# Kernel tuning notes

Hardware: AMD Instinct MI355X
Metric: run time of the kernel (lower is better)

Reference implementation:

```python
import jax, jax.numpy as jnp
import numpy as np

# Config from Hyperparameters / __init__ args
B, S, D = 2, 2048, 512
H, KV, HD = 8, 4, 64          # num_heads, num_kv_heads, head_dim = D // H
ROPE_BASE = 10000.0
QK_GAIN_INIT = 1.5
EPS = 1e-6


def setup_inputs() -> dict:
    key = jax.random.key(0)
    k0, k1, k2, k3, k4 = jax.random.split(key, 5)
    std = 0.02
    return {
        "x": jax.random.normal(k0, (B, S, D), dtype=jnp.float32),
        "wq": jax.random.normal(k1, (H * HD, D), dtype=jnp.float32) * std,
        "wk": jax.random.normal(k2, (KV * HD, D), dtype=jnp.float32) * std,
        "wv": jax.random.normal(k3, (KV * HD, D), dtype=jnp.float32) * std,
        "wo": jax.random.normal(k4, (D, H * HD), dtype=jnp.float32) * std,
        "qk_gain": jnp.asarray(QK_GAIN_INIT, dtype=jnp.float32),
    }


def _rope_tables(seq_len, head_dim, base, dtype):
    inv_freq = 1.0 / (base ** (jnp.arange(0, head_dim, 2, dtype=jnp.float32) / head_dim))
    t = jnp.arange(seq_len, dtype=jnp.float32)
    freqs = t[:, None] * inv_freq[None, :]              # [S, HD/2]
    return jnp.cos(freqs).astype(dtype)[None, None], jnp.sin(freqs).astype(dtype)[None, None]


def _apply_rotary(x, cos, sin):
    # matches apply_rotary_emb: split halves, rotate
    half = x.shape[-1] // 2
    x1, x2 = x[..., :half], x[..., half:]
    return jnp.concatenate([x1 * cos + x2 * sin, x1 * (-sin) + x2 * cos], axis=-1)


def _rms_norm(u):
    return u * jax.lax.rsqrt(jnp.mean(u * u, axis=-1, keepdims=True) + EPS)


def reference(x, wq, wk, wv, wo, qk_gain):
    b, s, d = x.shape
    # fused-style QKV projections (CastedLinear, no bias)
    q = (x @ wq.T).reshape(b, s, H, HD).transpose(0, 2, 1, 3)    # [B,H,S,HD]
    k = (x @ wk.T).reshape(b, s, KV, HD).transpose(0, 2, 1, 3)   # [B,KV,S,HD]
    v = (x @ wv.T).reshape(b, s, KV, HD).transpose(0, 2, 1, 3)   # [B,KV,S,HD]

    cos, sin = _rope_tables(s, HD, ROPE_BASE, x.dtype)
    q = _apply_rotary(q, cos, sin)
    k = _apply_rotary(k, cos, sin)

    # QK RMS-norm with learnable gain (init 1.5) on q
    q = _rms_norm(q) * qk_gain
    k = _rms_norm(k)

    # GQA: expand KV heads to H query heads
    rep = H // KV
    k = jnp.repeat(k, rep, axis=1)   # [B,H,S,HD]
    v = jnp.repeat(v, rep, axis=1)

    scale = 1.0 / np.sqrt(HD)
    scores = jnp.einsum("bhqd,bhkd->bhqk", q, k) * scale         # [B,H,S,S]
    causal = jnp.tril(jnp.ones((s, s), dtype=bool))
    scores = jnp.where(causal, scores, jnp.finfo(scores.dtype).min)
    attn = jax.nn.softmax(scores, axis=-1)
    out = jnp.einsum("bhqk,bhkd->bhqd", attn, v)                 # [B,H,S,HD]
    out = out.transpose(0, 2, 1, 3).reshape(b, s, H * HD)
    return out @ wo.T
```

## Files before the change

### kernel.cpp

```cpp
#include <hip/hip_runtime.h>
#include <math.h>

#define B_ 2
#define S_ 2048
#define D_ 512
#define H_ 8
#define KV_ 4
#define HD_ 64

typedef __attribute__((ext_vector_type(8))) short bf16x8;
typedef __attribute__((ext_vector_type(4))) short bf16x4;
typedef __attribute__((ext_vector_type(4))) float f32x4;
typedef __attribute__((ext_vector_type(16))) float f32x16;
typedef __attribute__((ext_vector_type(4))) unsigned u32x4;

static __device__ __forceinline__ unsigned short f2bf(float f) {
    union { float f; unsigned u; } v; v.f = f;
    unsigned r = v.u + 0x7FFFu + ((v.u >> 16) & 1);
    return (unsigned short)(r >> 16);
}

__global__ __launch_bounds__(256) void convert_pack_kernel(
    const float* __restrict__ x, const float* __restrict__ wq, const float* __restrict__ wk,
    const float* __restrict__ wv, const float* __restrict__ wo,
    unsigned short* __restrict__ xb, unsigned short* __restrict__ wqkv_b,
    unsigned short* __restrict__ wo_b, float* __restrict__ cosT, float* __restrict__ sinT) {
    if (blockIdx.x >= 2816) {
        int idx = (blockIdx.x - 2816) * 256 + threadIdx.x;
        int s = idx >> 5;
        int i = idx & 31;
        float invf = 1.0f / powf(10000.0f, (float)(2 * i) / (float)HD_);
        double a = (double)((float)s * invf);
        cosT[idx] = (float)cos(a);
        sinT[idx] = (float)sin(a);
        return;
    }
    int i4 = blockIdx.x * blockDim.x + threadIdx.x;
    int e = i4 * 4;
    const float* src;
    unsigned short* dst;
    if (e < 2097152)      { src = x + e;               dst = xb + e; }
    else if (e < 2359296) { src = wq + (e - 2097152);  dst = wqkv_b + (e - 2097152); }
    else if (e < 2490368) { src = wk + (e - 2359296);  dst = wqkv_b + (e - 2097152); }
    else if (e < 2621440) { src = wv + (e - 2490368);  dst = wqkv_b + (e - 2097152); }
    else                  { src = wo + (e - 2621440);  dst = wo_b + (e - 2621440); }
    float4 v = *(const float4*)src;
    bf16x4 o;
    o[0] = (short)f2bf(v.x); o[1] = (short)f2bf(v.y);
    o[2] = (short)f2bf(v.z); o[3] = (short)f2bf(v.w);
    *(bf16x4*)dst = o;
}

template <int EPI, typename OutT>
__global__ __launch_bounds__(256) void gemm_mfma(
    const unsigned short* __restrict__ A, const unsigned short* __restrict__ Bw,
    OutT* __restrict__ Y, int K, int ldy,
    const float* __restrict__ cosT, const float* __restrict__ sinT,
    const float* __restrict__ gainp) {
    __shared__ unsigned short As[128 * 32];
    __shared__ unsigned short Bs[128 * 32];
    const int bn = blockIdx.x * 128;
    const int bm = blockIdx.y * 128;
    const int t = threadIdx.x;
    const int w = t >> 6, l = t & 63;
    const int g = l >> 4, c = l & 15;
    const int wr = w >> 1, wc = w & 1;
    f32x4 acc[4][4] = {};
    const int lrow = l >> 2;
    const int lcol = (l & 3) * 8;
    for (int k0 = 0; k0 < K; k0 += 32) {
#pragma unroll
        for (int r = 0; r < 2; ++r) {
            int ci = w * 2 + r;
            const unsigned short* ga = A + (size_t)(bm + ci * 16 + lrow) * K + k0 + lcol;
            __builtin_amdgcn_global_load_lds(
                (const __attribute__((address_space(1))) void*)ga,
                (__attribute__((address_space(3))) void*)(As + ci * 512), 16, 0, 0);
            const unsigned short* gb = Bw + (size_t)(bn + ci * 16 + lrow) * K + k0 + lcol;
            __builtin_amdgcn_global_load_lds(
                (const __attribute__((address_space(1))) void*)gb,
                (__attribute__((address_space(3))) void*)(Bs + ci * 512), 16, 0, 0);
        }
        __syncthreads();
        bf16x8 av[4], bv[4];
#pragma unroll
        for (int i = 0; i < 4; ++i)
            av[i] = *(const bf16x8*)(As + (wr * 64 + i * 16 + c) * 32 + g * 8);
#pragma unroll
        for (int j = 0; j < 4; ++j)
            bv[j] = *(const bf16x8*)(Bs + (wc * 64 + j * 16 + c) * 32 + g * 8);
#pragma unroll
        for (int i = 0; i < 4; ++i)
#pragma unroll
            for (int j = 0; j < 4; ++j)
                acc[i][j] = __builtin_amdgcn_mfma_f32_16x16x32_bf16(av[i], bv[j], acc[i][j], 0, 0, 0);
        __syncthreads();
    }
    if constexpr (EPI == 2) {
        const float gv = *gainp;
        const float hscale = ((bn + wc * 64) < 512) ? gv : 1.0f;
#pragma unroll
        for (int i = 0; i < 4; ++i) {
#pragma unroll
            for (int r = 0; r < 4; ++r) {
                int row = bm + wr * 64 + i * 16 + g * 4 + r;
                int s = row & (S_ - 1);
                float c0 = cosT[s * 32 + c],      s0 = sinT[s * 32 + c];
                float c1 = cosT[s * 32 + c + 16], s1 = sinT[s * 32 + c + 16];
                float x1a = acc[i][0][r], x1b = acc[i][1][r];
                float x2a = acc[i][2][r], x2b = acc[i][3][r];
                float y1a = x1a * c0 + x2a * s0, y2a = x2a * c0 - x1a * s0;
                float y1b = x1b * c1 + x2b * s1, y2b = x2b * c1 - x1b * s1;
                float ss = y1a * y1a + y2a * y2a + y1b * y1b + y2b * y2b;
                ss += __shfl_xor(ss, 1, 64);
                ss += __shfl_xor(ss, 2, 64);
                ss += __shfl_xor(ss, 4, 64);
                ss += __shfl_xor(ss, 8, 64);
                float sc = rsqrtf(ss * (1.0f / 64.0f) + 1e-6f) * hscale;
                unsigned short* yr = (unsigned short*)Y + (size_t)row * ldy + bn + wc * 64 + c;
                yr[0]  = f2bf(y1a * sc);
                yr[16] = f2bf(y1b * sc);
                yr[32] = f2bf(y2a * sc);
                yr[48] = f2bf(y2b * sc);
            }
        }
    } else {
#pragma unroll
        for (int i = 0; i < 4; ++i)
#pragma unroll
            for (int j = 0; j < 4; ++j)
#pragma unroll
                for (int r = 0; r < 4; ++r) {
                    int row = bm + wr * 64 + i * 16 + g * 4 + r;
                    int col = bn + wc * 64 + j * 16 + c;
                    float v = acc[i][j][r];
                    if constexpr (EPI == 1)
                        Y[(size_t)row * ldy + col] = (OutT)f2bf(v);
                    else
                        Y[(size_t)row * ldy + col] = v;
                }
    }
}

#define SWZF(row) ((((row) + ((row) >> 3)) & 7) << 4)

__global__ __launch_bounds__(256, 3) void attn_mfma(const unsigned short* __restrict__ qkv,
                                                    const unsigned short* __restrict__ vt,
                                                    unsigned short* __restrict__ aout) {
    __shared__ alignas(128) char smem[32768];

    const int bid = blockIdx.x;
    const int bh = bid & 15;
    const int qt = 31 - (bid >> 4);
    const int hh = bh & 7;
    const int b = bh >> 3;
    const int kvh = hh >> 1;

    const int t = threadIdx.x;
    const int w = t >> 6;
    const int l = t & 63;
    const int wq = w >> 1;
    const int wk = w & 1;
    const int hl = l >> 5;
    const int l31 = l & 31;

    const int row0 = t >> 3;
    const int row1 = (256 + t) >> 3;
    const int seg = l & 7;
    const int off0 = (seg * 16) ^ SWZF(row0);
    const int off1 = (seg * 16) ^ SWZF(row1);
    const int cb0 = w * 1024;
    const int cb1 = 4096 + w * 1024;

    bf16x8 qf[4];
    {
        const unsigned short* qrow =
            qkv + (size_t)(b * S_ + qt * 64 + wq * 32 + l31) * 768 + hh * 64 + hl * 8;
#pragma unroll
        for (int kd = 0; kd < 4; ++kd)
            qf[kd] = *(const bf16x8*)(qrow + kd * 16);
    }

    const char* kb = (const char*)qkv + ((size_t)(b * S_)) * 1536 + 1024 + kvh * 128;
    const char* vb = (const char*)vt + ((size_t)(kvh * 64)) * 8192 + (size_t)(b * S_) * 2;

#define STAGE(kt_, bufi_)                                                                        \
    do {                                                                                         \
        const char* ks_ = kb + (size_t)(kt_) * 64 * 1536;                                        \
        const char* vs_ = vb + (size_t)(kt_) * 128;                                              \
        char* kd_ = smem + (bufi_)*8192;                                                         \
        char* vd_ = smem + 16384 + (bufi_)*8192;                                                 \
        __builtin_amdgcn_global_load_lds(                                                        \
            (const __attribute__((address_space(1))) void*)(ks_ + (size_t)row0 * 1536 + off0),   \
            (__attribute__((address_space(3))) void*)(kd_ + cb0), 16, 0, 0);                     \
        __builtin_amdgcn_global_load_lds(                                                        \
            (const __attribute__((address_space(1))) void*)(ks_ + (size_t)row1 * 1536 + off1),   \
            (__attribute__((address_space(3))) void*)(kd_ + cb1), 16, 0, 0);                     \
        __builtin_amdgcn_global_load_lds(                                                        \
            (const __attribute__((address_space(1))) void*)(vs_ + (size_t)row0 * 8192 + off0),   \
            (__attribute__((address_space(3))) void*)(vd_ + cb0), 16, 0, 0);                     \
        __builtin_amdgcn_global_load_lds(                                                        \
            (const __attribute__((address_space(1))) void*)(vs_ + (size_t)row1 * 8192 + off1),   \
            (__attribute__((address_space(3))) void*)(vd_ + cb1), 16, 0, 0);                     \
    } while (0)

    STAGE(0, 0);
    __syncthreads();

    float l_part = 0.0f;
    f32x16 o_acc[2] = {};
    const float LS = 0.125f * 1.4426950408889634f;
    const float SH = 6.0f * 1.4426950408889634f;

    int buf = 0;
    for (int kt = 0; kt <= qt; ++kt) {
        if (kt < qt) STAGE(kt + 1, buf ^ 1);
        const char* KsB = smem + buf * 8192;
        const char* VtB = smem + 16384 + buf * 8192;
        const bool diag = (kt == qt);

        if (!(diag && wk > wq)) {
            f32x16 s_acc = {};
            {
                int arow = wk * 32 + l31;
                int af = SWZF(arow);
                __builtin_amdgcn_s_setprio(1);
#pragma unroll
                for (int kd = 0; kd < 4; ++kd) {
                    bf16x8 afr = *(const bf16x8*)(KsB + arow * 128 + ((kd * 32 + hl * 16) ^ af));
                    s_acc = __builtin_amdgcn_mfma_f32_32x32x16_bf16(afr, qf[kd], s_acc, 0, 0, 0);
                }
                __builtin_amdgcn_s_setprio(0);
            }
            bf16x8 vf[2][2];
#pragma unroll
            for (int nd = 0; nd < 2; ++nd) {
                int vr = nd * 32 + l31;
                int fv = SWZF(vr);
#pragma unroll
                for (int m = 0; m < 2; ++m)
                    vf[nd][m] = *(const bf16x8*)(VtB + vr * 128 + ((wk * 64 + m * 32 + hl * 16) ^ fv));
            }
            float p[16];
            if (diag && wk == wq) {
#pragma unroll
                for (int idx = 0; idx < 16; ++idx) {
                    int keyin = 4 * hl + 8 * (idx >> 2) + (idx & 3);
                    float e = exp2f(s_acc[idx] * LS - SH);
                    p[idx] = (keyin <= l31) ? e : 0.0f;
                }
            } else {
#pragma unroll
                for (int idx = 0; idx < 16; ++idx)
                    p[idx] = exp2f(s_acc[idx] * LS - SH);
            }
#pragma unroll
            for (int idx = 0; idx < 16; ++idx) l_part += p[idx];
            unsigned pw[8];
#pragma unroll
            for (int s = 0; s < 4; ++s)
#pragma unroll
                for (int j = 0; j < 2; ++j)
                    asm("v_cvt_pk_bf16_f32 %0, %1, %2"
                        : "=v"(pw[s * 2 + j])
                        : "v"(p[4 * s + 2 * j]), "v"(p[4 * s + 2 * j + 1]));
#pragma unroll
            for (int m = 0; m < 2; ++m) {
                asm volatile("v_permlane32_swap_b32 %0, %1" : "+v"(pw[4 * m + 0]), "+v"(pw[4 * m + 2]));
                asm volatile("v_permlane32_swap_b32 %0, %1" : "+v"(pw[4 * m + 1]), "+v"(pw[4 * m + 3]));
            }
            __builtin_amdgcn_s_setprio(1);
#pragma unroll
            for (int m = 0; m < 2; ++m) {
                u32x4 fu = {pw[4 * m + 0], pw[4 * m + 1], pw[4 * m + 2], pw[4 * m + 3]};
                bf16x8 pfr = *(bf16x8*)&fu;
#pragma unroll
                for (int nd = 0; nd < 2; ++nd)
                    o_acc[nd] = __builtin_amdgcn_mfma_f32_32x32x16_bf16(pfr, vf[nd][m], o_acc[nd], 0, 0, 0);
            }
            __builtin_amdgcn_s_setprio(0);
        }
        __syncthreads();
        buf ^= 1;
    }
#undef STAGE

    float* Os = (float*)smem;
    float* Ls = (float*)(smem + 16384);
    float lsum = l_part + __shfl_xor(l_part, 32, 64);
    if (hl == 0) Ls[wk * 64 + wq * 32 + l31] = lsum;
    if (wk == 0) {
#pragma unroll
        for (int nd = 0; nd < 2; ++nd)
#pragma unroll
            for (int reg = 0; reg < 16; ++reg) {
                int qrow = 4 * hl + 8 * (reg >> 2) + (reg & 3);
                Os[(wq * 32 + qrow) * 64 + nd * 32 + l31] = o_acc[nd][reg];
            }
    }
    __syncthreads();
    if (wk == 1) {
        unsigned short* ob = aout + ((size_t)(b * S_ + qt * 64 + wq * 32)) * 512 + hh * 64;
#pragma unroll
        for (int reg = 0; reg < 16; ++reg) {
            int qrow = 4 * hl + 8 * (reg >> 2) + (reg & 3);
            float ltot = Ls[wq * 32 + qrow] + Ls[64 + wq * 32 + qrow];
            float inv = __builtin_amdgcn_rcpf(ltot);
#pragma unroll
            for (int nd = 0; nd < 2; ++nd) {
                float val = (o_acc[nd][reg] + Os[(wq * 32 + qrow) * 64 + nd * 32 + l31]) * inv;
                ob[(size_t)qrow * 512 + nd * 32 + l31] = f2bf(val);
            }
        }
    }
}

extern "C" void kernel_launch(void* const* d_in, const int* in_sizes, int n_in,
                              void* d_out, int out_size, void* d_ws, size_t ws_size,
                              hipStream_t stream) {
    const float* x    = (const float*)d_in[0];
    const float* wq   = (const float*)d_in[1];
    const float* wk   = (const float*)d_in[2];
    const float* wv   = (const float*)d_in[3];
    const float* wo   = (const float*)d_in[4];
    const float* gain = (const float*)d_in[5];
    float* out = (float*)d_out;

    char* ws = (char*)d_ws;
    unsigned short* qkv    = (unsigned short*)(ws);
    unsigned short* vt     = (unsigned short*)(ws + (size_t)6  * 1024 * 1024);
    unsigned short* aout   = (unsigned short*)(ws + (size_t)8  * 1024 * 1024);
    unsigned short* xb     = (unsigned short*)(ws + (size_t)12 * 1024 * 1024);
    unsigned short* wqkv_b = (unsigned short*)(ws + (size_t)16 * 1024 * 1024);
    unsigned short* wo_b   = (unsigned short*)(ws + (size_t)17 * 1024 * 1024);
    float* cosT            = (float*)(ws + (size_t)18 * 1024 * 1024);
    float* sinT            = cosT + (size_t)S_ * (HD_ / 2);

    convert_pack_kernel<<<3072, 256, 0, stream>>>(x, wq, wk, wv, wo, xb, wqkv_b, wo_b,
                                                  cosT, sinT);
    gemm_mfma<2, unsigned short><<<dim3(6, 32), 256, 0, stream>>>(
        xb, wqkv_b, qkv, 512, 768, cosT, sinT, gain);
    gemm_mfma<1, unsigned short><<<dim3(32, 2), 256, 0, stream>>>(
        wqkv_b + 768 * 512, xb, vt, 512, 4096, nullptr, nullptr, nullptr);
    attn_mfma<<<16 * (S_ / 64), 256, 0, stream>>>(qkv, vt, aout);
    gemm_mfma<0, float><<<dim3(4, 32), 256, 0, stream>>>(
        aout, wo_b, out, 512, 512, nullptr, nullptr, nullptr);
}
```

Measured before the change: 79.16 us.

## Split causal attention KV range into chunks and merge QKV/V-transpose GEMM launches

Attention work for each query tile is split into chunks of up to 8 KV tiles, so long causal rows run across several blocks. Partial unnormalized outputs and row sums go to a workspace, and a new combine kernel adds them and normalizes. The softmax shift is fixed, so partials can be summed directly. The QKV GEMM and the V-transpose GEMM are merged into one launch, which removes a launch and lets both fill the GPU together. In exchange there is extra fp32 partial traffic and an additional kernel launch.

```diff
diff --git a/kernel.cpp b/kernel.cpp
--- a/kernel.cpp
+++ b/kernel.cpp
@@ -52,15 +52,12 @@
 }
 
 template <int EPI, typename OutT>
-__global__ __launch_bounds__(256) void gemm_mfma(
+static __device__ __forceinline__ void gemm_body(
     const unsigned short* __restrict__ A, const unsigned short* __restrict__ Bw,
-    OutT* __restrict__ Y, int K, int ldy,
+    OutT* __restrict__ Y, int K, int ldy, int bn, int bm,
+    unsigned short* As, unsigned short* Bs,
     const float* __restrict__ cosT, const float* __restrict__ sinT,
     const float* __restrict__ gainp) {
-    __shared__ unsigned short As[128 * 32];
-    __shared__ unsigned short Bs[128 * 32];
-    const int bn = blockIdx.x * 128;
-    const int bm = blockIdx.y * 128;
     const int t = threadIdx.x;
     const int w = t >> 6, l = t & 63;
     const int g = l >> 4, c = l & 15;
@@ -142,16 +139,52 @@
     }
 }
 
+__global__ __launch_bounds__(256) void gemm_proj_fused(
+    const unsigned short* __restrict__ xb, const unsigned short* __restrict__ wqkv_b,
+    unsigned short* __restrict__ qkv, unsigned short* __restrict__ vt,
+    const float* __restrict__ cosT, const float* __restrict__ sinT,
+    const float* __restrict__ gainp) {
+    __shared__ unsigned short As[128 * 32];
+    __shared__ unsigned short Bs[128 * 32];
+    int bid = blockIdx.x;
+    if (bid < 192) {
+        int bx = bid % 6, by = bid / 6;
+        gemm_body<2, unsigned short>(xb, wqkv_b, qkv, 512, 768, bx * 128, by * 128,
+                                     As, Bs, cosT, sinT, gainp);
+    } else {
+        int b2 = bid - 192;
+        int bx = b2 & 31, by = b2 >> 5;
+        gemm_body<1, unsigned short>(wqkv_b + 768 * 512, xb, vt, 512, 4096, bx * 128, by * 128,
+                                     As, Bs, nullptr, nullptr, nullptr);
+    }
+}
+
+__global__ __launch_bounds__(256) void gemm_out(
+    const unsigned short* __restrict__ A, const unsigned short* __restrict__ Bw,
+    float* __restrict__ Y) {
+    __shared__ unsigned short As[128 * 32];
+    __shared__ unsigned short Bs[128 * 32];
+    gemm_body<0, float>(A, Bw, Y, 512, 512, blockIdx.x % 4 * 128, blockIdx.x / 4 * 128,
+                        As, Bs, nullptr, nullptr, nullptr);
+}
+
 #define SWZF(row) ((((row) + ((row) >> 3)) & 7) << 4)
 
 __global__ __launch_bounds__(256, 3) void attn_mfma(const unsigned short* __restrict__ qkv,
                                                     const unsigned short* __restrict__ vt,
-                                                    unsigned short* __restrict__ aout) {
+                                                    unsigned short* __restrict__ aout,
+                                                    float* __restrict__ pO,
+                                                    float* __restrict__ pL) {
     __shared__ alignas(128) char smem[32768];
 
-    const int bid = blockIdx.x;
-    const int bh = bid & 15;
-    const int qt = 31 - (bid >> 4);
+    const int slot = blockIdx.x >> 4;
+    const int bh = blockIdx.x & 15;
+    int qt = 31, acc = 0;
+    while (acc + (qt >> 3) + 1 <= slot) { acc += (qt >> 3) + 1; --qt; }
+    const int part = slot - acc;
+    const int np = (qt >> 3) + 1;
+    const int kt0 = part * 8;
+    const int kt1 = min(kt0 + 8, qt + 1);
     const int hh = bh & 7;
     const int b = bh >> 3;
     const int kvh = hh >> 1;
@@ -204,7 +237,7 @@
             (__attribute__((address_space(3))) void*)(vd_ + cb1), 16, 0, 0);                     \
     } while (0)
 
-    STAGE(0, 0);
+    STAGE(kt0, 0);
     __syncthreads();
 
     float l_part = 0.0f;
@@ -213,8 +246,8 @@
     const float SH = 6.0f * 1.4426950408889634f;
 
     int buf = 0;
-    for (int kt = 0; kt <= qt; ++kt) {
-        if (kt < qt) STAGE(kt + 1, buf ^ 1);
+    for (int kt = kt0; kt < kt1; ++kt) {
+        if (kt + 1 < kt1) STAGE(kt + 1, buf ^ 1);
         const char* KsB = smem + buf * 8192;
         const char* VtB = smem + 16384 + buf * 8192;
         const bool diag = (kt == qt);
@@ -300,18 +333,73 @@
     }
     __syncthreads();
     if (wk == 1) {
-        unsigned short* ob = aout + ((size_t)(b * S_ + qt * 64 + wq * 32)) * 512 + hh * 64;
-#pragma unroll
-        for (int reg = 0; reg < 16; ++reg) {
-            int qrow = 4 * hl + 8 * (reg >> 2) + (reg & 3);
-            float ltot = Ls[wq * 32 + qrow] + Ls[64 + wq * 32 + qrow];
-            float inv = __builtin_amdgcn_rcpf(ltot);
-#pragma unroll
-            for (int nd = 0; nd < 2; ++nd) {
-                float val = (o_acc[nd][reg] + Os[(wq * 32 + qrow) * 64 + nd * 32 + l31]) * inv;
-                ob[(size_t)qrow * 512 + nd * 32 + l31] = f2bf(val);
+        if (np == 1) {
+            unsigned short* ob = aout + ((size_t)(b * S_ + qt * 64 + wq * 32)) * 512 + hh * 64;
+#pragma unroll
+            for (int reg = 0; reg < 16; ++reg) {
+                int qrow = 4 * hl + 8 * (reg >> 2) + (reg & 3);
+                float ltot = Ls[wq * 32 + qrow] + Ls[64 + wq * 32 + qrow];
+                float inv = __builtin_amdgcn_rcpf(ltot);
+#pragma unroll
+                for (int nd = 0; nd < 2; ++nd) {
+                    float val = (o_acc[nd][reg] + Os[(wq * 32 + qrow) * 64 + nd * 32 + l31]) * inv;
+                    ob[(size_t)qrow * 512 + nd * 32 + l31] = f2bf(val);
+                }
+            }
+        } else {
+            float* po = pO + (size_t)blockIdx.x * 4096;
+            float* pl = pL + (size_t)blockIdx.x * 64;
+#pragma unroll
+            for (int reg = 0; reg < 16; ++reg) {
+                int qrow = 4 * hl + 8 * (reg >> 2) + (reg & 3);
+                float ltot = Ls[wq * 32 + qrow] + Ls[64 + wq * 32 + qrow];
+                if (l31 == 0) pl[wq * 32 + qrow] = ltot;
+#pragma unroll
+                for (int nd = 0; nd < 2; ++nd)
+                    po[(wq * 32 + qrow) * 64 + nd * 32 + l31] =
+                        o_acc[nd][reg] + Os[(wq * 32 + qrow) * 64 + nd * 32 + l31];
             }
         }
+    }
+}
+
+__global__ __launch_bounds__(256) void combine_kernel(const float* __restrict__ pO,
+                                                      const float* __restrict__ pL,
+                                                      unsigned short* __restrict__ aout) {
+    const int cid = blockIdx.x;
+    const int bh = cid & 15;
+    const int qt = 31 - (cid >> 4);
+    int qq = 31, acc = 0;
+    while (qq > qt) { acc += (qq >> 3) + 1; --qq; }
+    const int np = (qt >> 3) + 1;
+    const int base = acc * 16 + bh;
+    const int t = threadIdx.x;
+    const int row = t >> 2;
+    const int c0 = (t & 3) * 16;
+    float l = 0.0f;
+    float o[16] = {};
+    for (int p = 0; p < np; ++p) {
+        const int pid = base + p * 16;
+        l += pL[(size_t)pid * 64 + row];
+        const float* po = pO + (size_t)pid * 4096 + row * 64 + c0;
+#pragma unroll
+        for (int j4 = 0; j4 < 4; ++j4) {
+            float4 v = *(const float4*)(po + j4 * 4);
+            o[j4 * 4 + 0] += v.x; o[j4 * 4 + 1] += v.y;
+            o[j4 * 4 + 2] += v.z; o[j4 * 4 + 3] += v.w;
+        }
+    }
+    float inv = __builtin_amdgcn_rcpf(l);
+    const int b = bh >> 3, hh = bh & 7;
+    unsigned short* ob = aout + (size_t)(b * S_ + qt * 64 + row) * 512 + hh * 64 + c0;
+    bf16x4 pk[4];
+#pragma unroll
+    for (int j4 = 0; j4 < 4; ++j4) {
+        pk[j4][0] = (short)f2bf(o[j4 * 4 + 0] * inv);
+        pk[j4][1] = (short)f2bf(o[j4 * 4 + 1] * inv);
+        pk[j4][2] = (short)f2bf(o[j4 * 4 + 2] * inv);
+        pk[j4][3] = (short)f2bf(o[j4 * 4 + 3] * inv);
+        *(bf16x4*)(ob + j4 * 4) = pk[j4];
     }
 }
 
@@ -335,14 +423,13 @@
     unsigned short* wo_b   = (unsigned short*)(ws + (size_t)17 * 1024 * 1024);
     float* cosT            = (float*)(ws + (size_t)18 * 1024 * 1024);
     float* sinT            = cosT + (size_t)S_ * (HD_ / 2);
+    float* pO              = (float*)(ws + (size_t)32 * 1024 * 1024);
+    float* pL              = pO + (size_t)1280 * 4096;
 
     convert_pack_kernel<<<3072, 256, 0, stream>>>(x, wq, wk, wv, wo, xb, wqkv_b, wo_b,
                                                   cosT, sinT);
-    gemm_mfma<2, unsigned short><<<dim3(6, 32), 256, 0, stream>>>(
-        xb, wqkv_b, qkv, 512, 768, cosT, sinT, gain);
-    gemm_mfma<1, unsigned short><<<dim3(32, 2), 256, 0, stream>>>(
-        wqkv_b + 768 * 512, xb, vt, 512, 4096, nullptr, nullptr, nullptr);
-    attn_mfma<<<16 * (S_ / 64), 256, 0, stream>>>(qkv, vt, aout);
-    gemm_mfma<0, float><<<dim3(4, 32), 256, 0, stream>>>(
-        aout, wo_b, out, 512, 512, nullptr, nullptr, nullptr);
-}
+    gemm_proj_fused<<<256, 256, 0, stream>>>(xb, wqkv_b, qkv, vt, cosT, sinT, gain);
+    attn_mfma<<<1280, 256, 0, stream>>>(qkv, vt, aout, pO, pL);
+    combine_kernel<<<384, 256, 0, stream>>>(pO, pL, aout);
+    gemm_out<<<128, 256, 0, stream>>>(aout, wo_b, out);
+}
```

Measured after the change: 68.23 us. -13.8%, faster.
